# Optimization experiments

Measured on AMD Instinct MI355X. Metric: run time of the kernel, lower is better.

The kernel has to match this reference:

```python
import jax, jax.numpy as jnp
import numpy as np

B, S, R, H = 256, 196, 1024, 512  # batch, att regions, rnn_size, att_hid_size


def setup_inputs() -> dict:
    key = jax.random.key(0)
    ks = jax.random.split(key, 8)
    return {
        "att_feats": jax.random.normal(ks[0], (B, S, R), dtype=jnp.float32),
        "p_att_feats": jax.random.normal(ks[1], (B, S, H), dtype=jnp.float32),
        "hidden": jax.random.normal(ks[2], (B, R), dtype=jnp.float32),
        "in_weights": jax.random.uniform(ks[3], (B, S), dtype=jnp.float32),
        "h2att_w": jax.random.normal(ks[4], (H, R), dtype=jnp.float32) * (1.0 / np.sqrt(R)),
        "h2att_b": jnp.full((H,), 0.1, dtype=jnp.float32),
        "alpha_w": jax.random.normal(ks[5], (1, H), dtype=jnp.float32) * (1.0 / np.sqrt(H)),
        "alpha_b": jnp.full((1,), 0.1, dtype=jnp.float32),
    }


def reference(att_feats, p_att_feats, hidden, in_weights, h2att_w, h2att_b, alpha_w, alpha_b):
    # att = in_weights * p_att_feats          [B, S, H]
    att = in_weights[:, :, None] * p_att_feats
    # att_h = h2att(hidden)                   [B, H] broadcast over S
    att_h = hidden @ h2att_w.T + h2att_b
    dot = jnp.tanh(att + att_h[:, None, :])   # [B, S, H]
    # alpha_net: Linear(H, 1) -> scores       [B, S]
    scores = jnp.einsum('bsh,h->bs', dot, alpha_w[0]) + alpha_b[0]
    weight = jax.nn.softmax(scores, axis=-1)  # [B, S]
    # weighted pooling: bmm(weight[:,None,:], att_feats).squeeze(1)
    att_res = jnp.einsum('bs,bsr->br', weight, att_feats)  # [B, R]
    return (att_res, weight)
```

## Files before the change

kernel.cpp:

```cpp
#include <hip/hip_runtime.h>

#define BN 256
#define SN 196
#define RN 1024
#define HN 512

__device__ __forceinline__ float fast_tanh(float x) {
    float e = __expf(2.0f * x);
    return 1.0f - 2.0f * __builtin_amdgcn_rcpf(e + 1.0f);
}

__global__ __launch_bounds__(256) void k_att_h(
    const float* __restrict__ hidden, const float* __restrict__ w,
    const float* __restrict__ bias, float* __restrict__ att_h) {
    __shared__ float As[16][68];
    __shared__ float Bs[32][68];
    const int t  = threadIdx.x;
    const int h0 = blockIdx.x * 32;
    const int b0 = blockIdx.y * 16;
    const int tx = t & 31;
    const int ty = t >> 5;
    const int ar = t >> 4, ac = (t & 15) << 2;
    float acc0 = 0.f, acc1 = 0.f;

    for (int k0 = 0; k0 < RN; k0 += 64) {
        float4 av = *(const float4*)(hidden + (size_t)(b0 + ar) * RN + k0 + ac);
        *(float4*)(&As[ar][ac]) = av;
#pragma unroll
        for (int j = 0; j < 2; j++) {
            int idx = t + j * 256;
            int br = idx >> 4, bc = (idx & 15) << 2;
            float4 bv = *(const float4*)(w + (size_t)(h0 + br) * RN + k0 + bc);
            *(float4*)(&Bs[br][bc]) = bv;
        }
        __syncthreads();
#pragma unroll
        for (int k = 0; k < 64; k++) {
            float bb = Bs[tx][k];
            acc0 = fmaf(As[ty][k],     bb, acc0);
            acc1 = fmaf(As[ty + 8][k], bb, acc1);
        }
        __syncthreads();
    }
    float bsc = bias[h0 + tx];
    att_h[(size_t)(b0 + ty)     * HN + h0 + tx] = acc0 + bsc;
    att_h[(size_t)(b0 + ty + 8) * HN + h0 + tx] = acc1 + bsc;
}

__global__ __launch_bounds__(256) void k_scores(
    const float* __restrict__ p_att, const float* __restrict__ in_w,
    const float* __restrict__ att_h, const float* __restrict__ alpha_w,
    const float* __restrict__ alpha_b, float* __restrict__ scores) {
    const int lane = threadIdx.x & 63;
    const int gid  = blockIdx.x * 4 + (threadIdx.x >> 6);
    const int b    = gid / SN;

    const float iw = in_w[gid];
    const float4* p4 = (const float4*)(p_att + (size_t)gid * HN);
    const float4* a4 = (const float4*)(alpha_w);
    const float4* h4 = (const float4*)(att_h + (size_t)b * HN);

    float sum = 0.f;
#pragma unroll
    for (int i = 0; i < 2; i++) {
        int idx = lane + i * 64;
        float4 p  = p4[idx];
        float4 aw = a4[idx];
        float4 ah = h4[idx];
        sum += fast_tanh(fmaf(iw, p.x, ah.x)) * aw.x;
        sum += fast_tanh(fmaf(iw, p.y, ah.y)) * aw.y;
        sum += fast_tanh(fmaf(iw, p.z, ah.z)) * aw.z;
        sum += fast_tanh(fmaf(iw, p.w, ah.w)) * aw.w;
    }
#pragma unroll
    for (int off = 32; off > 0; off >>= 1)
        sum += __shfl_xor(sum, off, 64);
    if (lane == 0) scores[gid] = sum + alpha_b[0];
}

__global__ __launch_bounds__(64) void k_softmax(float* __restrict__ wout) {
    const int b    = blockIdx.x;
    const int lane = threadIdx.x;
    float* row = wout + (size_t)b * SN;

    float vals[4];
    float m = -1e30f;
#pragma unroll
    for (int i = 0; i < 4; i++) {
        int s = lane + i * 64;
        vals[i] = (s < SN) ? row[s] : -1e30f;
        m = fmaxf(m, vals[i]);
    }
#pragma unroll
    for (int off = 32; off > 0; off >>= 1)
        m = fmaxf(m, __shfl_xor(m, off, 64));

    float e[4];
    float sum = 0.f;
#pragma unroll
    for (int i = 0; i < 4; i++) {
        int s = lane + i * 64;
        e[i] = (s < SN) ? __expf(vals[i] - m) : 0.f;
        sum += e[i];
    }
#pragma unroll
    for (int off = 32; off > 0; off >>= 1)
        sum += __shfl_xor(sum, off, 64);

    float inv = __builtin_amdgcn_rcpf(sum);
#pragma unroll
    for (int i = 0; i < 4; i++) {
        int s = lane + i * 64;
        if (s < SN) row[s] = e[i] * inv;
    }
}

__global__ __launch_bounds__(128) void k_pool(
    const float* __restrict__ att_feats, const float* __restrict__ weight,
    float* __restrict__ att_res) {
    __shared__ float w[SN];
    const int b    = blockIdx.x >> 1;
    const int half = blockIdx.x & 1;
    const int t    = threadIdx.x;

    for (int s = t; s < SN; s += 128) w[s] = weight[(size_t)b * SN + s];
    __syncthreads();

    const int r0 = half * 512 + t * 4;
    const float* base = att_feats + (size_t)b * SN * RN + r0;
    float4 acc = make_float4(0.f, 0.f, 0.f, 0.f);

    for (int s = 0; s < SN; s += 4) {
        float4 v0 = *(const float4*)(base + (size_t)(s    ) * RN);
        float4 v1 = *(const float4*)(base + (size_t)(s + 1) * RN);
        float4 v2 = *(const float4*)(base + (size_t)(s + 2) * RN);
        float4 v3 = *(const float4*)(base + (size_t)(s + 3) * RN);
        float w0 = w[s], w1 = w[s + 1], w2 = w[s + 2], w3 = w[s + 3];
        acc.x += w0 * v0.x + w1 * v1.x + w2 * v2.x + w3 * v3.x;
        acc.y += w0 * v0.y + w1 * v1.y + w2 * v2.y + w3 * v3.y;
        acc.z += w0 * v0.z + w1 * v1.z + w2 * v2.z + w3 * v3.z;
        acc.w += w0 * v0.w + w1 * v1.w + w2 * v2.w + w3 * v3.w;
    }
    *(float4*)(att_res + (size_t)b * RN + r0) = acc;
}

extern "C" void kernel_launch(void* const* d_in, const int* in_sizes, int n_in,
                              void* d_out, int out_size, void* d_ws, size_t ws_size,
                              hipStream_t stream) {
    const float* att_feats   = (const float*)d_in[0];
    const float* p_att_feats = (const float*)d_in[1];
    const float* hidden      = (const float*)d_in[2];
    const float* in_weights  = (const float*)d_in[3];
    const float* h2att_w     = (const float*)d_in[4];
    const float* h2att_b     = (const float*)d_in[5];
    const float* alpha_w     = (const float*)d_in[6];
    const float* alpha_b     = (const float*)d_in[7];

    float* att_res = (float*)d_out;
    float* weight  = (float*)d_out + BN * RN;
    float* att_h   = (float*)d_ws;

    k_att_h  <<<dim3(HN / 32, BN / 16), 256, 0, stream>>>(hidden, h2att_w, h2att_b, att_h);
    k_scores <<<(BN * SN) / 4, 256, 0, stream>>>(p_att_feats, in_weights, att_h,
                                                 alpha_w, alpha_b, weight);
    k_softmax<<<BN, 64, 0, stream>>>(weight);
    k_pool   <<<BN * 2, 128, 0, stream>>>(att_feats, weight, att_res);
}
```

Before: 383.0 us.

## Split-K register-tiled h2att GEMM and fuse scores, softmax and pooling per batch

Replaces the small-tile att_h GEMM with a 64x64 register-tiled split-K GEMM that writes partial sums. The three remaining kernels become one per-batch kernel with 1024 threads. That kernel reduces the partials plus the bias in shared memory, computes the scores, runs the softmax in shared memory and does the weighted pooling with a cross-wave reduction. This removes launches and global round trips for att_h and the scores, and raises GEMM arithmetic intensity. It adds an 8 MB partial buffer, and using one block per batch limits parallelism to 256 blocks. alpha_b is dropped because softmax is shift-invariant.

```diff
diff --git a/kernel.cpp b/kernel.cpp
--- a/kernel.cpp
+++ b/kernel.cpp
@@ -1,147 +1,169 @@
 #include <hip/hip_runtime.h>
+#include <math.h>
 
 #define BN 256
 #define SN 196
 #define RN 1024
 #define HN 512
+#define KSPLIT 16
+#define KCH 64
 
 __device__ __forceinline__ float fast_tanh(float x) {
     float e = __expf(2.0f * x);
     return 1.0f - 2.0f * __builtin_amdgcn_rcpf(e + 1.0f);
 }
 
-__global__ __launch_bounds__(256) void k_att_h(
+__global__ __launch_bounds__(256) void k_gemm_partial(
     const float* __restrict__ hidden, const float* __restrict__ w,
-    const float* __restrict__ bias, float* __restrict__ att_h) {
-    __shared__ float As[16][68];
-    __shared__ float Bs[32][68];
+    float* __restrict__ partial) {
+    __shared__ float At[KCH][64];
+    __shared__ float Bt[KCH][64];
     const int t  = threadIdx.x;
-    const int h0 = blockIdx.x * 32;
-    const int b0 = blockIdx.y * 16;
-    const int tx = t & 31;
-    const int ty = t >> 5;
-    const int ar = t >> 4, ac = (t & 15) << 2;
-    float acc0 = 0.f, acc1 = 0.f;
+    const int b0 = blockIdx.x * 64;
+    const int h0 = blockIdx.y * 64;
+    const int kc = blockIdx.z;
+    const int k0 = kc * KCH;
 
-    for (int k0 = 0; k0 < RN; k0 += 64) {
-        float4 av = *(const float4*)(hidden + (size_t)(b0 + ar) * RN + k0 + ac);
-        *(float4*)(&As[ar][ac]) = av;
+    {
+        const int row = t >> 2, kq = (t & 3) * 16;
+        const float* srcA = hidden + (size_t)(b0 + row) * RN + k0 + kq;
+        const float* srcB = w      + (size_t)(h0 + row) * RN + k0 + kq;
 #pragma unroll
-        for (int j = 0; j < 2; j++) {
-            int idx = t + j * 256;
-            int br = idx >> 4, bc = (idx & 15) << 2;
-            float4 bv = *(const float4*)(w + (size_t)(h0 + br) * RN + k0 + bc);
-            *(float4*)(&Bs[br][bc]) = bv;
+        for (int j = 0; j < 4; ++j) {
+            float4 v = *(const float4*)(srcA + j * 4);
+            int k = kq + j * 4;
+            At[k][row] = v.x; At[k + 1][row] = v.y; At[k + 2][row] = v.z; At[k + 3][row] = v.w;
         }
-        __syncthreads();
 #pragma unroll
-        for (int k = 0; k < 64; k++) {
-            float bb = Bs[tx][k];
-            acc0 = fmaf(As[ty][k],     bb, acc0);
-            acc1 = fmaf(As[ty + 8][k], bb, acc1);
+        for (int j = 0; j < 4; ++j) {
+            float4 v = *(const float4*)(srcB + j * 4);
+            int k = kq + j * 4;
+            Bt[k][row] = v.x; Bt[k + 1][row] = v.y; Bt[k + 2][row] = v.z; Bt[k + 3][row] = v.w;
         }
-        __syncthreads();
     }
-    float bsc = bias[h0 + tx];
-    att_h[(size_t)(b0 + ty)     * HN + h0 + tx] = acc0 + bsc;
-    att_h[(size_t)(b0 + ty + 8) * HN + h0 + tx] = acc1 + bsc;
+    __syncthreads();
+
+    const int th4 = (t & 15) * 4;
+    const int tb4 = (t >> 4) * 4;
+    float4 acc0 = {0,0,0,0}, acc1 = {0,0,0,0}, acc2 = {0,0,0,0}, acc3 = {0,0,0,0};
+#pragma unroll 8
+    for (int k = 0; k < KCH; ++k) {
+        float4 a  = *(const float4*)&At[k][tb4];
+        float4 bb = *(const float4*)&Bt[k][th4];
+        acc0.x = fmaf(a.x, bb.x, acc0.x); acc0.y = fmaf(a.x, bb.y, acc0.y);
+        acc0.z = fmaf(a.x, bb.z, acc0.z); acc0.w = fmaf(a.x, bb.w, acc0.w);
+        acc1.x = fmaf(a.y, bb.x, acc1.x); acc1.y = fmaf(a.y, bb.y, acc1.y);
+        acc1.z = fmaf(a.y, bb.z, acc1.z); acc1.w = fmaf(a.y, bb.w, acc1.w);
+        acc2.x = fmaf(a.z, bb.x, acc2.x); acc2.y = fmaf(a.z, bb.y, acc2.y);
+        acc2.z = fmaf(a.z, bb.z, acc2.z); acc2.w = fmaf(a.z, bb.w, acc2.w);
+        acc3.x = fmaf(a.w, bb.x, acc3.x); acc3.y = fmaf(a.w, bb.y, acc3.y);
+        acc3.z = fmaf(a.w, bb.z, acc3.z); acc3.w = fmaf(a.w, bb.w, acc3.w);
+    }
+    float* dst = partial + ((size_t)kc * BN + b0 + tb4) * HN + h0 + th4;
+    *(float4*)(dst)          = acc0;
+    *(float4*)(dst + HN)     = acc1;
+    *(float4*)(dst + 2 * HN) = acc2;
+    *(float4*)(dst + 3 * HN) = acc3;
 }
 
-__global__ __launch_bounds__(256) void k_scores(
+__global__ __launch_bounds__(1024) void k_fused(
+    const float* __restrict__ partial, const float* __restrict__ bias,
     const float* __restrict__ p_att, const float* __restrict__ in_w,
-    const float* __restrict__ att_h, const float* __restrict__ alpha_w,
-    const float* __restrict__ alpha_b, float* __restrict__ scores) {
-    const int lane = threadIdx.x & 63;
-    const int gid  = blockIdx.x * 4 + (threadIdx.x >> 6);
-    const int b    = gid / SN;
+    const float* __restrict__ alpha_w, const float* __restrict__ att_feats,
+    float* __restrict__ att_res, float* __restrict__ weight_out) {
+    __shared__ float att_h[HN];
+    __shared__ float sc[256];
+    __shared__ float red[16 * 256];
+    const int b    = blockIdx.x;
+    const int t    = threadIdx.x;
+    const int wv   = t >> 6;
+    const int lane = t & 63;
 
-    const float iw = in_w[gid];
-    const float4* p4 = (const float4*)(p_att + (size_t)gid * HN);
-    const float4* a4 = (const float4*)(alpha_w);
-    const float4* h4 = (const float4*)(att_h + (size_t)b * HN);
+    if (t >= SN && t < 256) sc[t] = -1e30f;
 
-    float sum = 0.f;
+    if (t < 128) {
+        float4 s = *(const float4*)(bias + t * 4);
+        const float* p = partial + (size_t)b * HN + t * 4;
 #pragma unroll
-    for (int i = 0; i < 2; i++) {
-        int idx = lane + i * 64;
-        float4 p  = p4[idx];
-        float4 aw = a4[idx];
-        float4 ah = h4[idx];
-        sum += fast_tanh(fmaf(iw, p.x, ah.x)) * aw.x;
-        sum += fast_tanh(fmaf(iw, p.y, ah.y)) * aw.y;
-        sum += fast_tanh(fmaf(iw, p.z, ah.z)) * aw.z;
-        sum += fast_tanh(fmaf(iw, p.w, ah.w)) * aw.w;
+        for (int kc = 0; kc < KSPLIT; ++kc) {
+            float4 v = *(const float4*)(p + (size_t)kc * BN * HN);
+            s.x += v.x; s.y += v.y; s.z += v.z; s.w += v.w;
+        }
+        *(float4*)&att_h[t * 4] = s;
     }
-#pragma unroll
-    for (int off = 32; off > 0; off >>= 1)
-        sum += __shfl_xor(sum, off, 64);
-    if (lane == 0) scores[gid] = sum + alpha_b[0];
-}
-
-__global__ __launch_bounds__(64) void k_softmax(float* __restrict__ wout) {
-    const int b    = blockIdx.x;
-    const int lane = threadIdx.x;
-    float* row = wout + (size_t)b * SN;
-
-    float vals[4];
-    float m = -1e30f;
-#pragma unroll
-    for (int i = 0; i < 4; i++) {
-        int s = lane + i * 64;
-        vals[i] = (s < SN) ? row[s] : -1e30f;
-        m = fmaxf(m, vals[i]);
-    }
-#pragma unroll
-    for (int off = 32; off > 0; off >>= 1)
-        m = fmaxf(m, __shfl_xor(m, off, 64));
-
-    float e[4];
-    float sum = 0.f;
-#pragma unroll
-    for (int i = 0; i < 4; i++) {
-        int s = lane + i * 64;
-        e[i] = (s < SN) ? __expf(vals[i] - m) : 0.f;
-        sum += e[i];
-    }
-#pragma unroll
-    for (int off = 32; off > 0; off >>= 1)
-        sum += __shfl_xor(sum, off, 64);
-
-    float inv = __builtin_amdgcn_rcpf(sum);
-#pragma unroll
-    for (int i = 0; i < 4; i++) {
-        int s = lane + i * 64;
-        if (s < SN) row[s] = e[i] * inv;
-    }
-}
-
-__global__ __launch_bounds__(128) void k_pool(
-    const float* __restrict__ att_feats, const float* __restrict__ weight,
-    float* __restrict__ att_res) {
-    __shared__ float w[SN];
-    const int b    = blockIdx.x >> 1;
-    const int half = blockIdx.x & 1;
-    const int t    = threadIdx.x;
-
-    for (int s = t; s < SN; s += 128) w[s] = weight[(size_t)b * SN + s];
     __syncthreads();
 
-    const int r0 = half * 512 + t * 4;
-    const float* base = att_feats + (size_t)b * SN * RN + r0;
-    float4 acc = make_float4(0.f, 0.f, 0.f, 0.f);
+    {
+        const float4* a4 = (const float4*)alpha_w;
+        float4 aw0 = a4[lane], aw1 = a4[lane + 64];
+        float4 ah0 = *(const float4*)&att_h[lane * 4];
+        float4 ah1 = *(const float4*)&att_h[(lane + 64) * 4];
+        const float4* p4 = (const float4*)p_att;
+        for (int si = wv; si < SN; si += 16) {
+            float  iw = in_w[b * SN + si];
+            size_t rb = (size_t)(b * SN + si) * (HN / 4);
+            float4 p0 = p4[rb + lane];
+            float4 p1 = p4[rb + lane + 64];
+            float sum;
+            sum  = fast_tanh(fmaf(iw, p0.x, ah0.x)) * aw0.x;
+            sum += fast_tanh(fmaf(iw, p0.y, ah0.y)) * aw0.y;
+            sum += fast_tanh(fmaf(iw, p0.z, ah0.z)) * aw0.z;
+            sum += fast_tanh(fmaf(iw, p0.w, ah0.w)) * aw0.w;
+            sum += fast_tanh(fmaf(iw, p1.x, ah1.x)) * aw1.x;
+            sum += fast_tanh(fmaf(iw, p1.y, ah1.y)) * aw1.y;
+            sum += fast_tanh(fmaf(iw, p1.z, ah1.z)) * aw1.z;
+            sum += fast_tanh(fmaf(iw, p1.w, ah1.w)) * aw1.w;
+#pragma unroll
+            for (int off = 32; off; off >>= 1) sum += __shfl_xor(sum, off, 64);
+            if (lane == 0) sc[si] = sum;
+        }
+    }
+    __syncthreads();
 
-    for (int s = 0; s < SN; s += 4) {
-        float4 v0 = *(const float4*)(base + (size_t)(s    ) * RN);
-        float4 v1 = *(const float4*)(base + (size_t)(s + 1) * RN);
-        float4 v2 = *(const float4*)(base + (size_t)(s + 2) * RN);
-        float4 v3 = *(const float4*)(base + (size_t)(s + 3) * RN);
-        float w0 = w[s], w1 = w[s + 1], w2 = w[s + 2], w3 = w[s + 3];
-        acc.x += w0 * v0.x + w1 * v1.x + w2 * v2.x + w3 * v3.x;
-        acc.y += w0 * v0.y + w1 * v1.y + w2 * v2.y + w3 * v3.y;
-        acc.z += w0 * v0.z + w1 * v1.z + w2 * v2.z + w3 * v3.z;
-        acc.w += w0 * v0.w + w1 * v1.w + w2 * v2.w + w3 * v3.w;
+    if (wv == 0) {
+        float v0 = sc[lane], v1 = sc[lane + 64], v2 = sc[lane + 128], v3 = sc[lane + 192];
+        float m = fmaxf(fmaxf(v0, v1), fmaxf(v2, v3));
+#pragma unroll
+        for (int off = 32; off; off >>= 1) m = fmaxf(m, __shfl_xor(m, off, 64));
+        float e0 = __expf(v0 - m), e1 = __expf(v1 - m);
+        float e2 = __expf(v2 - m), e3 = __expf(v3 - m);
+        float s = e0 + e1 + e2 + e3;
+#pragma unroll
+        for (int off = 32; off; off >>= 1) s += __shfl_xor(s, off, 64);
+        float inv = 1.0f / s;
+        e0 *= inv; e1 *= inv; e2 *= inv; e3 *= inv;
+        sc[lane] = e0; sc[lane + 64] = e1; sc[lane + 128] = e2; sc[lane + 192] = e3;
+        float* wo = weight_out + (size_t)b * SN;
+        wo[lane] = e0; wo[lane + 64] = e1; wo[lane + 128] = e2;
+        if (lane + 192 < SN) wo[lane + 192] = e3;
     }
-    *(float4*)(att_res + (size_t)b * RN + r0) = acc;
+    __syncthreads();
+
+    {
+        const int g = wv >> 2, q = wv & 3;
+        const float* base = att_feats + (size_t)b * SN * RN + q * 256 + lane * 4;
+        float4 acc = {0,0,0,0};
+        for (int i = 0; i < 49; i += 7) {
+#pragma unroll
+            for (int j = 0; j < 7; ++j) {
+                int s = g + 4 * (i + j);
+                float ws = sc[s];
+                float4 v = *(const float4*)(base + (size_t)s * RN);
+                acc.x = fmaf(ws, v.x, acc.x);
+                acc.y = fmaf(ws, v.y, acc.y);
+                acc.z = fmaf(ws, v.z, acc.z);
+                acc.w = fmaf(ws, v.w, acc.w);
+            }
+        }
+        *(float4*)&red[wv * 256 + lane * 4] = acc;
+    }
+    __syncthreads();
+    {
+        const int q2 = t >> 8, rr = t & 255;
+        float r = red[q2 * 256 + rr] + red[(4 + q2) * 256 + rr]
+                + red[(8 + q2) * 256 + rr] + red[(12 + q2) * 256 + rr];
+        att_res[(size_t)b * RN + t] = r;
+    }
 }
 
 extern "C" void kernel_launch(void* const* d_in, const int* in_sizes, int n_in,
@@ -154,15 +176,13 @@
     const float* h2att_w     = (const float*)d_in[4];
     const float* h2att_b     = (const float*)d_in[5];
     const float* alpha_w     = (const float*)d_in[6];
-    const float* alpha_b     = (const float*)d_in[7];
 
     float* att_res = (float*)d_out;
     float* weight  = (float*)d_out + BN * RN;
-    float* att_h   = (float*)d_ws;
+    float* partial = (float*)d_ws;
 
-    k_att_h  <<<dim3(HN / 32, BN / 16), 256, 0, stream>>>(hidden, h2att_w, h2att_b, att_h);
-    k_scores <<<(BN * SN) / 4, 256, 0, stream>>>(p_att_feats, in_weights, att_h,
-                                                 alpha_w, alpha_b, weight);
-    k_softmax<<<BN, 64, 0, stream>>>(weight);
-    k_pool   <<<BN * 2, 128, 0, stream>>>(att_feats, weight, att_res);
+    k_gemm_partial<<<dim3(BN / 64, HN / 64, KSPLIT), 256, 0, stream>>>(
+        hidden, h2att_w, partial);
+    k_fused<<<BN, 1024, 0, stream>>>(partial, h2att_b, p_att_feats, in_weights,
+                                     alpha_w, att_feats, att_res, weight);
 }
```

Result: faster. 363.0 us (-5.2%).
